# Kernel optimization log

Hardware: AMD Instinct MI355X
Metric: run time of the kernel (lower is better)

## Reference

```python
import jax, jax.numpy as jnp
import numpy as np

N, D, H = 4096, 1024, 2048


def positional_encoding(d_model, n):
    even_i = jnp.arange(0, d_model, 2, dtype=jnp.float32)
    denom = jnp.power(jnp.float32(10000.0), even_i / d_model)
    pos = jnp.arange(n, dtype=jnp.float32)[:, None]            # (N,1)
    even_pe = jnp.sin(pos / denom)                             # (N,D/2)
    odd_pe = jnp.cos(pos / denom)                              # (N,D/2)
    # interleave sin/cos: stack on axis 2 then flatten -> (N, D)
    return jnp.stack([even_pe, odd_pe], axis=2).reshape(n, d_model)


def setup_inputs() -> dict:
    key = jax.random.key(0)
    ks = jax.random.split(key, 5)
    X = jax.random.normal(ks[0], (N, D), dtype=jnp.float32)
    mask = jnp.ones((N,), dtype=jnp.int32)  # unused by the module
    Wv = jax.random.normal(ks[1], (D, D), dtype=jnp.float32) * 0.02
    bv = jnp.zeros((D,), dtype=jnp.float32)
    W1 = jax.random.normal(ks[2], (2 * D, H), dtype=jnp.float32) * 0.02
    b1 = jnp.zeros((H,), dtype=jnp.float32)
    W2 = jax.random.normal(ks[3], (H, N), dtype=jnp.float32) * 0.02
    b2 = jnp.zeros((N,), dtype=jnp.float32)
    return {"X": X, "mask": mask, "Wv": Wv, "bv": bv,
            "W1": W1, "b1": b1, "W2": W2, "b2": b2}


def reference(X, mask, Wv, bv, W1, b1, W2, b2):
    n, d = X.shape
    V = X @ Wv + bv                                            # (N,D)
    PE = positional_encoding(d, n).astype(X.dtype)
    E = PE * X                                                 # (N,D)
    # leave-one-out mean: (global sum - row_i) / (N-1)  [replaces O(N^2) loop]
    loo = (jnp.sum(E, axis=0, keepdims=True) - E) / (n - 1)    # (N,D)
    feat = jnp.concatenate([X, loo], axis=1)                   # (N,2D)
    hidden = jax.nn.relu(feat @ W1 + b1)                       # (N,H)
    att_scores = hidden @ W2 + b2                              # (N,N)
    att_weights = jax.nn.softmax(att_scores, axis=-1)          # (N,N)
    # dropout p=0 (inference) -> identity
    return att_weights @ V                                     # (N,D)
```

## Files before the change

kernel.cpp:

```cpp
#include <hip/hip_runtime.h>
#include <hip/hip_bf16.h>

#define TOK 4096
#define DIM 1024
#define HID 2048
#define LN10K 9.210340371976184f

typedef __bf16 bh;
typedef __bf16 v8bf __attribute__((ext_vector_type(8)));
typedef float v4f __attribute__((ext_vector_type(4)));

typedef const __attribute__((address_space(1))) void* gvp;
typedef __attribute__((address_space(3))) void* svp;

__device__ __forceinline__ void gl_lds16(const bh* g, bh* s) {
  __builtin_amdgcn_global_load_lds((gvp)g, (svp)s, 16, 0, 0);
}

__global__ __launch_bounds__(256) void prep_x_colsum(const float* __restrict__ X,
                                                     bh* __restrict__ featb,
                                                     float* __restrict__ S) {
  int cp = blockIdx.x * 256 + threadIdx.x;
  int c = cp * 2;
  int r0 = blockIdx.y * 16;
  float inv_denom = __expf(-(float)c * (LN10K / (float)DIM));
  float s0 = 0.f, s1 = 0.f;
#pragma unroll 4
  for (int r = r0; r < r0 + 16; ++r) {
    float2 x = *(const float2*)(X + (size_t)r * DIM + c);
    float sn, cs;
    __sincosf((float)r * inv_denom, &sn, &cs);
    s0 += sn * x.x;
    s1 += cs * x.y;
    bh pair[2] = {(bh)x.x, (bh)x.y};
    *(ushort2*)(featb + (size_t)r * (2 * DIM) + c) = *(ushort2*)pair;
  }
  atomicAdd(&S[c], s0);
  atomicAdd(&S[c + 1], s1);
}

__global__ __launch_bounds__(256) void prep_loo(const float* __restrict__ X,
                                                const float* __restrict__ S,
                                                bh* __restrict__ featb) {
  size_t e4 = ((size_t)blockIdx.x * 256 + threadIdx.x) * 4;
  int r = (int)(e4 >> 10);
  int c = (int)(e4 & 1023);
  float4 x = *(const float4*)(X + e4);
  float4 s = *(const float4*)(S + c);
  float id0 = __expf(-(float)c * (LN10K / (float)DIM));
  float id1 = __expf(-(float)(c + 2) * (LN10K / (float)DIM));
  float sn0, cs0, sn1, cs1;
  __sincosf((float)r * id0, &sn0, &cs0);
  __sincosf((float)r * id1, &sn1, &cs1);
  const float inv = 1.0f / (float)(TOK - 1);
  bh outv[4];
  outv[0] = (bh)((s.x - sn0 * x.x) * inv);
  outv[1] = (bh)((s.y - cs0 * x.y) * inv);
  outv[2] = (bh)((s.z - sn1 * x.z) * inv);
  outv[3] = (bh)((s.w - cs1 * x.w) * inv);
  *(ushort4*)(featb + (size_t)r * (2 * DIM) + DIM + c) = *(ushort4*)outv;
}

__global__ __launch_bounds__(256) void transpose_all(const float* __restrict__ Wv,
                                                     const float* __restrict__ W1,
                                                     const float* __restrict__ W2,
                                                     bh* __restrict__ WvT,
                                                     bh* __restrict__ W1T,
                                                     bh* __restrict__ W2T) {
  __shared__ float tile[32][33];
  int bid = blockIdx.x;
  const float* in; bh* out; int Ncol, R, bx, by;
  if (bid < 1024)      { in = Wv; out = WvT; Ncol = DIM; R = DIM;
                         bx = bid & 31; by = bid >> 5; }
  else if (bid < 5120) { int b = bid - 1024; in = W1; out = W1T; Ncol = HID; R = 2 * DIM;
                         bx = b & 63; by = b >> 6; }
  else                 { int b = bid - 5120; in = W2; out = W2T; Ncol = TOK; R = HID;
                         bx = b & 127; by = b >> 7; }
  int nb = bx * 32, rb = by * 32;
  int tx = threadIdx.x, ty = threadIdx.y;
#pragma unroll
  for (int j = 0; j < 32; j += 8)
    tile[ty + j][tx] = in[(size_t)(rb + ty + j) * Ncol + nb + tx];
  __syncthreads();
#pragma unroll
  for (int j = 0; j < 32; j += 8)
    out[(size_t)(nb + ty + j) * R + rb + tx] = (bh)tile[tx][ty + j];
}

template <int BN, bool RELU, bool TROUT, bool EXPS, typename OutT>
__global__ __launch_bounds__(128, 2) void gemm_bt(const bh* __restrict__ A,
                                                  const bh* __restrict__ BT,
                                                  const float* __restrict__ bias,
                                                  OutT* __restrict__ C,
                                                  float* __restrict__ rowsum,
                                                  int K, int lda, int ldbt, int ldc) {
  constexpr int NT = BN / 16;
  __shared__ bh As[128 * 64];
  __shared__ bh Bs[BN * 64];
  const int t = threadIdx.x;
  const int id = blockIdx.x;
  const int bm = (id & 31) * 128, bn = (id >> 5) * BN;

  const int sr = t >> 3;
  const int c8 = ((t & 7) ^ (sr & 7)) * 8;
  const bh* gA = A + (size_t)(bm + sr) * lda + c8;
  const bh* gB = BT + (size_t)(bn + sr) * ldbt + c8;
  bh* sA = As + t * 8;
  bh* sB = Bs + t * 8;

  const int lane = t & 63, w = t >> 6;
  const int lc = lane & 15, q = lane >> 4;

  v4f acc[4][NT] = {};
  for (int k0 = 0; k0 < K; k0 += 64) {
#pragma unroll
    for (int j = 0; j < 8; ++j)
      gl_lds16(gA + k0 + j * 16 * lda, sA + j * 1024);
#pragma unroll
    for (int j = 0; j < NT; ++j)
      gl_lds16(gB + k0 + j * 16 * ldbt, sB + j * 1024);
    __syncthreads();
#pragma unroll
    for (int h = 0; h < 2; ++h) {
      const int off = ((h * 4 + q) ^ (lc & 7)) * 8;
      v8bf af[4], bfr[NT];
#pragma unroll
      for (int mt = 0; mt < 4; ++mt)
        af[mt] = *(const v8bf*)(As + (w * 64 + mt * 16 + lc) * 64 + off);
#pragma unroll
      for (int nt = 0; nt < NT; ++nt)
        bfr[nt] = *(const v8bf*)(Bs + (nt * 16 + lc) * 64 + off);
#pragma unroll
      for (int mt = 0; mt < 4; ++mt)
#pragma unroll
        for (int nt = 0; nt < NT; ++nt)
          acc[mt][nt] = __builtin_amdgcn_mfma_f32_16x16x32_bf16(af[mt], bfr[nt], acc[mt][nt], 0, 0, 0);
    }
    __syncthreads();
  }

  const int r4 = q * 4;
  if (EXPS) {
    float bbv[NT];
#pragma unroll
    for (int nt = 0; nt < NT; ++nt) bbv[nt] = bias ? bias[bn + nt * 16 + lc] : 0.0f;
#pragma unroll
    for (int mt = 0; mt < 4; ++mt) {
#pragma unroll
      for (int r = 0; r < 4; ++r) {
        int row = bm + w * 64 + mt * 16 + r4 + r;
        float rs = 0.0f;
#pragma unroll
        for (int nt = 0; nt < NT; ++nt) {
          float val = __expf(acc[mt][nt][r] + bbv[nt]);
          rs += val;
          C[(size_t)row * ldc + bn + nt * 16 + lc] = (OutT)val;
        }
        rs += __shfl_xor(rs, 1);
        rs += __shfl_xor(rs, 2);
        rs += __shfl_xor(rs, 4);
        rs += __shfl_xor(rs, 8);
        if (lc == 0) atomicAdd(rowsum + row, rs);
      }
    }
  } else {
#pragma unroll
    for (int mt = 0; mt < 4; ++mt) {
      int row0 = bm + w * 64 + mt * 16 + r4;
#pragma unroll
      for (int nt = 0; nt < NT; ++nt) {
        int col = bn + nt * 16 + lc;
        float bb = bias ? bias[col] : 0.0f;
#pragma unroll
        for (int r = 0; r < 4; ++r) {
          float val = acc[mt][nt][r] + bb;
          if (RELU) val = fmaxf(val, 0.0f);
          if (TROUT) C[(size_t)col * ldc + (row0 + r)] = (OutT)val;
          else       C[(size_t)(row0 + r) * ldc + col] = (OutT)val;
        }
      }
    }
  }
}

__global__ __launch_bounds__(256, 4) void gemm4_split(const bh* __restrict__ A,
                                                      const bh* __restrict__ BT,
                                                      float* __restrict__ C0,
                                                      float* __restrict__ C1) {
  __shared__ bh As[128 * 64];
  __shared__ bh Bs[128 * 64];
  const int t = threadIdx.x;
  const int id = blockIdx.x;
  const int bm = (id & 31) * 128, bn = (id >> 5) * 128;
  const int kbeg = blockIdx.y * (TOK / 2);

  const int sr = t >> 3;
  const int c8 = ((t & 7) ^ (sr & 7)) * 8;
  const bh* gA = A + (size_t)(bm + sr) * TOK + kbeg + c8;
  const bh* gB = BT + (size_t)(bn + sr) * TOK + kbeg + c8;
  bh* sA = As + t * 8;
  bh* sB = Bs + t * 8;

  const int lane = t & 63, w = t >> 6;
  const int wm = (w >> 1) * 64, wn = (w & 1) * 64;
  const int lc = lane & 15, q = lane >> 4;

  v4f acc[4][4] = {};
  for (int k0 = 0; k0 < TOK / 2; k0 += 64) {
#pragma unroll
    for (int j = 0; j < 4; ++j) {
      gl_lds16(gA + k0 + (size_t)(j * 32) * TOK, sA + j * 2048);
      gl_lds16(gB + k0 + (size_t)(j * 32) * TOK, sB + j * 2048);
    }
    __syncthreads();
#pragma unroll
    for (int h = 0; h < 2; ++h) {
      const int off = ((h * 4 + q) ^ (lc & 7)) * 8;
      v8bf af[4], bfr[4];
#pragma unroll
      for (int mt = 0; mt < 4; ++mt)
        af[mt] = *(const v8bf*)(As + (wm + mt * 16 + lc) * 64 + off);
#pragma unroll
      for (int nt = 0; nt < 4; ++nt)
        bfr[nt] = *(const v8bf*)(Bs + (wn + nt * 16 + lc) * 64 + off);
#pragma unroll
      for (int mt = 0; mt < 4; ++mt)
#pragma unroll
        for (int nt = 0; nt < 4; ++nt)
          acc[mt][nt] = __builtin_amdgcn_mfma_f32_16x16x32_bf16(af[mt], bfr[nt], acc[mt][nt], 0, 0, 0);
    }
    __syncthreads();
  }

  float* C = blockIdx.y ? C1 : C0;
  const int r4 = q * 4;
#pragma unroll
  for (int mt = 0; mt < 4; ++mt) {
    int row0 = bm + wm + mt * 16 + r4;
#pragma unroll
    for (int nt = 0; nt < 4; ++nt) {
      int col = bn + wn + nt * 16 + lc;
#pragma unroll
      for (int r = 0; r < 4; ++r)
        C[(size_t)(row0 + r) * DIM + col] = acc[mt][nt][r];
    }
  }
}

__global__ __launch_bounds__(256) void finalize(const float* __restrict__ p0,
                                                const float* __restrict__ p1,
                                                const float* __restrict__ rowsum,
                                                float* __restrict__ out) {
  size_t i = ((size_t)blockIdx.x * 256 + threadIdx.x) * 4;
  int row = (int)(i >> 10);
  float inv = 1.0f / rowsum[row];
  float4 a = *(const float4*)(p0 + i);
  float4 b = *(const float4*)(p1 + i);
  float4 o;
  o.x = (a.x + b.x) * inv; o.y = (a.y + b.y) * inv;
  o.z = (a.z + b.z) * inv; o.w = (a.w + b.w) * inv;
  *(float4*)(out + i) = o;
}

extern "C" void kernel_launch(void* const* d_in, const int* in_sizes, int n_in,
                              void* d_out, int out_size, void* d_ws, size_t ws_size,
                              hipStream_t stream) {
  (void)in_sizes; (void)n_in; (void)out_size; (void)ws_size;
  const float* X  = (const float*)d_in[0];
  const float* Wv = (const float*)d_in[2];
  const float* bv = (const float*)d_in[3];
  const float* W1 = (const float*)d_in[4];
  const float* b1 = (const float*)d_in[5];
  const float* W2 = (const float*)d_in[6];
  const float* b2 = (const float*)d_in[7];
  float* out = (float*)d_out;

  char* ws = (char*)d_ws;
  bh* featb = (bh*)(ws);
  bh* WvT   = (bh*)(ws + (16u << 20));
  bh* W1T   = (bh*)(ws + (18u << 20));
  bh* W2T   = (bh*)(ws + (26u << 20));
  bh* Vt    = (bh*)(ws + (42u << 20));
  bh* hid   = (bh*)(ws + (50u << 20));
  bh* scr   = (bh*)(ws + (66u << 20));
  float* S  = (float*)(ws + (98u << 20));
  float* rowsum = (float*)(ws + (98u << 20) + 4096);
  float* part0 = (float*)(ws);
  float* part1 = (float*)(ws + (26u << 20));

  hipError_t e = hipMemsetAsync(S, 0, 4096 + 4096 * sizeof(float), stream);
  (void)e;
  prep_x_colsum<<<dim3(DIM / 512, TOK / 16), 256, 0, stream>>>(X, featb, S);
  prep_loo<<<dim3((TOK * DIM) / 1024), 256, 0, stream>>>(X, S, featb);
  transpose_all<<<dim3(1024 + 4096 + 8192), dim3(32, 8), 0, stream>>>(
      Wv, W1, W2, WvT, W1T, W2T);

  gemm_bt<64, false, true, false, bh><<<dim3(32 * (DIM / 64)), 128, 0, stream>>>(
      featb, WvT, bv, Vt, nullptr, DIM, 2 * DIM, DIM, TOK);
  gemm_bt<128, true, false, false, bh><<<dim3(32 * (HID / 128)), 128, 0, stream>>>(
      featb, W1T, b1, hid, nullptr, 2 * DIM, 2 * DIM, 2 * DIM, HID);
  gemm_bt<128, false, false, true, bh><<<dim3(32 * (TOK / 128)), 128, 0, stream>>>(
      hid, W2T, b2, scr, rowsum, HID, HID, HID, TOK);
  gemm4_split<<<dim3(256, 2), 256, 0, stream>>>(scr, Vt, part0, part1);
  finalize<<<dim3((TOK * DIM) / 1024), 256, 0, stream>>>(part0, part1, rowsum, out);
}
```

Measured before the change: 322.2 us.

## Use 4-wave 2x2 warp tiling in gemm_bt and stage transposed output through LDS

gemm_bt now launches 256 threads arranged as a 2x2 grid of waves, so each wave computes half the N extent instead of all of it. This halves per-wave accumulator registers and adds waves per block to hide latency. The tile loads are respread across the extra threads. The transposed-output path (V^T) now writes through shared memory and stores 16-byte vectors, replacing scattered 2-byte column stores. The trade-off is more LDS traffic and an extra barrier in the epilogue.

Result: faster. 312.1 us (-3.1%).

```diff
diff --git a/kernel.cpp b/kernel.cpp
--- a/kernel.cpp
+++ b/kernel.cpp
@@ -88,37 +88,38 @@
 }
 
 template <int BN, bool RELU, bool TROUT, bool EXPS, typename OutT>
-__global__ __launch_bounds__(128, 2) void gemm_bt(const bh* __restrict__ A,
+__global__ __launch_bounds__(256, 2) void gemm_bt(const bh* __restrict__ A,
                                                   const bh* __restrict__ BT,
                                                   const float* __restrict__ bias,
                                                   OutT* __restrict__ C,
                                                   float* __restrict__ rowsum,
                                                   int K, int lda, int ldbt, int ldc) {
-  constexpr int NT = BN / 16;
+  constexpr int NT = BN / 32;
   __shared__ bh As[128 * 64];
   __shared__ bh Bs[BN * 64];
   const int t = threadIdx.x;
   const int id = blockIdx.x;
   const int bm = (id & 31) * 128, bn = (id >> 5) * BN;
 
-  const int sr = t >> 3;
-  const int c8 = ((t & 7) ^ (sr & 7)) * 8;
-  const bh* gA = A + (size_t)(bm + sr) * lda + c8;
-  const bh* gB = BT + (size_t)(bn + sr) * ldbt + c8;
+  const int srow = t >> 3;
+  const int c8 = ((t & 7) ^ (srow & 7)) * 8;
+  const bh* gA = A + (size_t)(bm + srow) * lda + c8;
+  const bh* gB = BT + (size_t)(bn + srow) * ldbt + c8;
   bh* sA = As + t * 8;
   bh* sB = Bs + t * 8;
 
   const int lane = t & 63, w = t >> 6;
+  const int wm = (w >> 1) * 64, wn = (w & 1) * (BN / 2);
   const int lc = lane & 15, q = lane >> 4;
 
   v4f acc[4][NT] = {};
   for (int k0 = 0; k0 < K; k0 += 64) {
 #pragma unroll
-    for (int j = 0; j < 8; ++j)
-      gl_lds16(gA + k0 + j * 16 * lda, sA + j * 1024);
-#pragma unroll
-    for (int j = 0; j < NT; ++j)
-      gl_lds16(gB + k0 + j * 16 * ldbt, sB + j * 1024);
+    for (int j = 0; j < 4; ++j)
+      gl_lds16(gA + k0 + j * 32 * lda, sA + j * 2048);
+#pragma unroll
+    for (int j = 0; j < BN / 32; ++j)
+      gl_lds16(gB + k0 + j * 32 * ldbt, sB + j * 2048);
     __syncthreads();
 #pragma unroll
     for (int h = 0; h < 2; ++h) {
@@ -126,10 +127,10 @@
       v8bf af[4], bfr[NT];
 #pragma unroll
       for (int mt = 0; mt < 4; ++mt)
-        af[mt] = *(const v8bf*)(As + (w * 64 + mt * 16 + lc) * 64 + off);
+        af[mt] = *(const v8bf*)(As + (wm + mt * 16 + lc) * 64 + off);
 #pragma unroll
       for (int nt = 0; nt < NT; ++nt)
-        bfr[nt] = *(const v8bf*)(Bs + (nt * 16 + lc) * 64 + off);
+        bfr[nt] = *(const v8bf*)(Bs + (wn + nt * 16 + lc) * 64 + off);
 #pragma unroll
       for (int mt = 0; mt < 4; ++mt)
 #pragma unroll
@@ -143,18 +144,19 @@
   if (EXPS) {
     float bbv[NT];
 #pragma unroll
-    for (int nt = 0; nt < NT; ++nt) bbv[nt] = bias ? bias[bn + nt * 16 + lc] : 0.0f;
+    for (int nt = 0; nt < NT; ++nt)
+      bbv[nt] = bias ? bias[bn + wn + nt * 16 + lc] : 0.0f;
 #pragma unroll
     for (int mt = 0; mt < 4; ++mt) {
 #pragma unroll
       for (int r = 0; r < 4; ++r) {
-        int row = bm + w * 64 + mt * 16 + r4 + r;
+        int row = bm + wm + mt * 16 + r4 + r;
         float rs = 0.0f;
 #pragma unroll
         for (int nt = 0; nt < NT; ++nt) {
           float val = __expf(acc[mt][nt][r] + bbv[nt]);
           rs += val;
-          C[(size_t)row * ldc + bn + nt * 16 + lc] = (OutT)val;
+          C[(size_t)row * ldc + bn + wn + nt * 16 + lc] = (OutT)val;
         }
         rs += __shfl_xor(rs, 1);
         rs += __shfl_xor(rs, 2);
@@ -163,20 +165,43 @@
         if (lc == 0) atomicAdd(rowsum + row, rs);
       }
     }
-  } else {
+  } else if (TROUT) {
+    bh* trs = As;
 #pragma unroll
     for (int mt = 0; mt < 4; ++mt) {
-      int row0 = bm + w * 64 + mt * 16 + r4;
 #pragma unroll
       for (int nt = 0; nt < NT; ++nt) {
-        int col = bn + nt * 16 + lc;
-        float bb = bias ? bias[col] : 0.0f;
+        int cl = wn + nt * 16 + lc;
+        float bb = bias ? bias[bn + cl] : 0.0f;
 #pragma unroll
         for (int r = 0; r < 4; ++r) {
           float val = acc[mt][nt][r] + bb;
           if (RELU) val = fmaxf(val, 0.0f);
-          if (TROUT) C[(size_t)col * ldc + (row0 + r)] = (OutT)val;
-          else       C[(size_t)(row0 + r) * ldc + col] = (OutT)val;
+          trs[cl * 128 + (wm + mt * 16 + r4 + r)] = (bh)val;
+        }
+      }
+    }
+    __syncthreads();
+#pragma unroll
+    for (int p = 0; p < 4; ++p) {
+      int chunk = p * 256 + t;
+      int vr = chunk >> 4, sc = chunk & 15;
+      *(v8bf*)((bh*)C + (size_t)(bn + vr) * ldc + bm + sc * 8) =
+          *(const v8bf*)(trs + vr * 128 + sc * 8);
+    }
+  } else {
+#pragma unroll
+    for (int mt = 0; mt < 4; ++mt) {
+      int row0 = bm + wm + mt * 16 + r4;
+#pragma unroll
+      for (int nt = 0; nt < NT; ++nt) {
+        int col = bn + wn + nt * 16 + lc;
+        float bb = bias ? bias[col] : 0.0f;
+#pragma unroll
+        for (int r = 0; r < 4; ++r) {
+          float val = acc[mt][nt][r] + bb;
+          if (RELU) val = fmaxf(val, 0.0f);
+          C[(size_t)(row0 + r) * ldc + col] = (OutT)val;
         }
       }
     }
@@ -295,11 +320,11 @@
   transpose_all<<<dim3(1024 + 4096 + 8192), dim3(32, 8), 0, stream>>>(
       Wv, W1, W2, WvT, W1T, W2T);
 
-  gemm_bt<64, false, true, false, bh><<<dim3(32 * (DIM / 64)), 128, 0, stream>>>(
+  gemm_bt<64, false, true, false, bh><<<dim3(32 * (DIM / 64)), 256, 0, stream>>>(
       featb, WvT, bv, Vt, nullptr, DIM, 2 * DIM, DIM, TOK);
-  gemm_bt<128, true, false, false, bh><<<dim3(32 * (HID / 128)), 128, 0, stream>>>(
+  gemm_bt<128, true, false, false, bh><<<dim3(32 * (HID / 128)), 256, 0, stream>>>(
       featb, W1T, b1, hid, nullptr, 2 * DIM, 2 * DIM, 2 * DIM, HID);
-  gemm_bt<128, false, false, true, bh><<<dim3(32 * (TOK / 128)), 128, 0, stream>>>(
+  gemm_bt<128, false, false, true, bh><<<dim3(32 * (TOK / 128)), 256, 0, stream>>>(
       hid, W2T, b2, scr, rowsum, HID, HID, HID, TOK);
   gemm4_split<<<dim3(256, 2), 256, 0, stream>>>(scr, Vt, part0, part1);
   finalize<<<dim3((TOK * DIM) / 1024), 256, 0, stream>>>(part0, part1, rowsum, out);
```
